# Kernel tuning notes

Hardware: AMD Instinct MI355X
Metric: run time of the kernel (lower is better)

Reference implementation:

```python
import jax, jax.numpy as jnp
import numpy as np

K = 4  # neighbors per node (loop=False, PyG knn_graph default)

def _leaky(x):
    return jax.nn.leaky_relu(x, negative_slope=0.01)

def _knn(pos):
    # pos: [B, N, 3]. k nearest neighbors per node within its own graph, no self-loops.
    d = jnp.sum((pos[:, :, None, :] - pos[:, None, :, :]) ** 2, axis=-1)  # [B, N, N]
    n = pos.shape[1]
    d = jnp.where(jnp.eye(n, dtype=bool), jnp.inf, d)
    _, idx = jax.lax.top_k(-d, K)
    return idx  # [B, N, K] neighbor (source) indices per center node

def _edge_conv(x, idx, w1, b1, w2, b2):
    # PyG EdgeConv, aggr='add': out_i = sum_j MLP(concat[x_i, x_j - x_i])
    xj = jax.vmap(lambda xb, ib: xb[ib])(x, idx)  # gather neighbors -> [B, N, K, F]
    xi = x[:, :, None, :]
    e = jnp.concatenate([jnp.broadcast_to(xi, xj.shape), xj - xi], axis=-1)  # [B,N,K,2F]
    h = _leaky(_leaky(e @ w1 + b1) @ w2 + b2)
    return h.sum(axis=2)  # scatter-add over the K neighbors -> [B, N, F_out]

# l1=4, l2=96, l3=192, l4=252, l5=192, l6=96, l7=1  (input_size=4, c=3, output_size=1)
PARAM_SHAPES = [
    ("c1w1", (8, 96)), ("c1b1", (96,)), ("c1w2", (96, 192)), ("c1b2", (192,)),
    ("c2w1", (384, 252)), ("c2b1", (252,)), ("c2w2", (252, 192)), ("c2b2", (192,)),
    ("c3w1", (384, 252)), ("c3b1", (252,)), ("c3w2", (252, 192)), ("c3b2", (192,)),
    ("c4w1", (384, 252)), ("c4b1", (252,)), ("c4w2", (252, 192)), ("c4b2", (192,)),
    ("nn1w", (772, 252)), ("nn1b", (252,)),
    ("nn2w", (252, 192)), ("nn2b", (192,)),
    ("nn3w", (768, 96)), ("nn3b", (96,)),
    ("nn4w", (96, 1)), ("nn4b", (1,)),
]

def setup_inputs():
    key = jax.random.key(0)
    B, N, F = 256, 256, 4  # 256 graphs x 256 nodes, 4 node features
    inp = {"x": jax.random.normal(key, (B, N, F), jnp.float32)}
    for i, (name, shp) in enumerate(PARAM_SHAPES):
        k = jax.random.fold_in(key, i + 1)
        scale = 1.0 / np.sqrt(shp[0]) if len(shp) == 2 else 0.01
        inp[name] = jax.random.normal(k, shp, jnp.float32) * scale
    return inp

def reference(x, c1w1, c1b1, c1w2, c1b2, c2w1, c2b1, c2w2, c2b2,
              c3w1, c3b1, c3w2, c3b2, c4w1, c4b1, c4w2, c4b2,
              nn1w, nn1b, nn2w, nn2b, nn3w, nn3b, nn4w, nn4b):
    # 4 rounds of (dynamic kNN on first 3 feature cols) + EdgeConv(add)
    a = _edge_conv(x, _knn(x[..., :3]), c1w1, c1b1, c1w2, c1b2)
    b = _edge_conv(a, _knn(a[..., :3]), c2w1, c2b1, c2w2, c2b2)
    c = _edge_conv(b, _knn(b[..., :3]), c3w1, c3b1, c3w2, c3b2)
    d = _edge_conv(c, _knn(c[..., :3]), c4w1, c4b1, c4w2, c4b2)
    h = jnp.concatenate([x, a, b, c, d], axis=-1)  # [B, N, 4 + 4*192 = 772]
    h = _leaky(h @ nn1w + nn1b)
    h = h @ nn2w + nn2b  # [B, N, 192]
    # four-way global pooling per graph: max / min / sum / mean
    pooled = jnp.concatenate(
        [h.max(axis=1), h.min(axis=1), h.sum(axis=1), h.mean(axis=1)], axis=-1)  # [B, 768]
    out = _leaky(pooled)
    out = _leaky(out @ nn3w + nn3b)
    return out @ nn4w + nn4b  # [B, 1] (mode='custom': no tanh)
```

## Files before the change

kernel.cpp:

```cpp
#include <hip/hip_runtime.h>
#include <cstdint>
#include <cstddef>

#define LK(x) ((x) > 0.f ? (x) : 0.01f * (x))

typedef _Float16 f16x8 __attribute__((ext_vector_type(8)));
typedef _Float16 f16x4 __attribute__((ext_vector_type(4)));
typedef float f32x4 __attribute__((ext_vector_type(4)));

constexpr int B_ = 256;
constexpr int N_ = 256;
constexpr int BN = B_ * N_;
constexpr int CHUNK_B = 64;
constexpr int CHUNK_ROWS = CHUNK_B * N_;

__device__ inline void dec2(float v, _Float16& h, _Float16& l) {
  _Float16 hh = (_Float16)v;
  h = hh;
  l = (_Float16)(v - (float)hh);
}

__global__ void knn_kernel(const float* __restrict__ feat, int F, int* __restrict__ idxout) {
  __shared__ float px[N_], py[N_], pz[N_];
  int b = blockIdx.x, t = threadIdx.x;
  const float* row = feat + ((size_t)b * N_ + t) * F;
  px[t] = row[0]; py[t] = row[1]; pz[t] = row[2];
  __syncthreads();
  float x = px[t], y = py[t], z = pz[t];
  float bd0 = INFINITY, bd1 = INFINITY, bd2 = INFINITY, bd3 = INFINITY;
  int bi0 = 0, bi1 = 0, bi2 = 0, bi3 = 0;
  for (int j = 0; j < N_; ++j) {
    #pragma clang fp contract(off)
    float dx = x - px[j], dy = y - py[j], dz = z - pz[j];
    float d = (dx * dx + dy * dy) + dz * dz;
    if (j == t) continue;
    if (d < bd3) {
      if (d < bd2) {
        bd3 = bd2; bi3 = bi2;
        if (d < bd1) {
          bd2 = bd1; bi2 = bi1;
          if (d < bd0) { bd1 = bd0; bi1 = bi0; bd0 = d; bi0 = j; }
          else         { bd1 = d; bi1 = j; }
        } else         { bd2 = d; bi2 = j; }
      } else           { bd3 = d; bi3 = j; }
    }
  }
  int* o = idxout + ((size_t)b * N_ + t) * 4;
  o[0] = bi0; o[1] = bi1; o[2] = bi2; o[3] = bi3;
}


__global__ void prep_uvw(const float* __restrict__ w1, const float* __restrict__ b1,
                         int F, int H1, float* __restrict__ wcat, float* __restrict__ bcat) {
  int t = blockIdx.x * 256 + threadIdx.x;
  int FH = F * H1;
  if (t < FH) {
    int k = t / H1, c = t - k * H1;
    float top = w1[(size_t)k * H1 + c];
    float bot = w1[(size_t)(F + k) * H1 + c];
    wcat[(size_t)k * 2 * H1 + c]      = top - bot;
    wcat[(size_t)k * 2 * H1 + H1 + c] = bot;
  }
  if (t < H1) { bcat[t] = b1[t]; bcat[H1 + t] = 0.f; }
}

template<bool ACT_A, bool ACCUM, bool HAS_BIAS>
__global__ __launch_bounds__(256) void gemm_f32(
    const float* __restrict__ A, const float* __restrict__ W,
    const float* __restrict__ bias, float* __restrict__ C,
    int M, int N, int K) {
  __shared__ float sA[16][132];
  __shared__ float sW[16][132];
  int tid = threadIdx.x;
  int m0 = blockIdx.y * 128;
  int n0 = blockIdx.x * 128;
  int kkA = tid & 15, mA = tid >> 4;
  int nW = tid & 127, kW = tid >> 7;
  int ty = tid >> 4, tx = tid & 15;
  float acc[8][8] = {};
  for (int k0 = 0; k0 < K; k0 += 16) {
    int kg = k0 + kkA;
    #pragma unroll
    for (int i = 0; i < 8; ++i) {
      int m = mA + i * 16;
      float v = 0.f;
      if (kg < K) {
        v = A[(size_t)(m0 + m) * K + kg];
        if (ACT_A) v = LK(v);
      }
      sA[kkA][m] = v;
    }
    #pragma unroll
    for (int q = 0; q < 8; ++q) {
      int kk = kW + q * 2;
      int kgw = k0 + kk, n = n0 + nW;
      float v = 0.f;
      if (kgw < K && n < N) v = W[(size_t)kgw * N + n];
      sW[kk][nW] = v;
    }
    __syncthreads();
    #pragma unroll
    for (int kk = 0; kk < 16; ++kk) {
      float4 a0 = *(const float4*)&sA[kk][ty * 8];
      float4 a1 = *(const float4*)&sA[kk][ty * 8 + 4];
      float4 w0 = *(const float4*)&sW[kk][tx * 4];
      float4 w1 = *(const float4*)&sW[kk][64 + tx * 4];
      float av[8] = {a0.x, a0.y, a0.z, a0.w, a1.x, a1.y, a1.z, a1.w};
      float wv[8] = {w0.x, w0.y, w0.z, w0.w, w1.x, w1.y, w1.z, w1.w};
      #pragma unroll
      for (int i = 0; i < 8; ++i)
        #pragma unroll
        for (int j = 0; j < 8; ++j)
          acc[i][j] += av[i] * wv[j];
    }
    __syncthreads();
  }
  #pragma unroll
  for (int h = 0; h < 2; ++h) {
    int n = n0 + h * 64 + tx * 4;
    float bv[4] = {0.f, 0.f, 0.f, 0.f};
    if (HAS_BIAS) {
      #pragma unroll
      for (int j = 0; j < 4; ++j) if (n + j < N) bv[j] = bias[n + j];
    }
    #pragma unroll
    for (int i = 0; i < 8; ++i) {
      size_t m = (size_t)(m0 + ty * 8 + i);
      if (n + 3 < N) {
        float4 o;
        o.x = acc[i][h * 4 + 0] + bv[0]; o.y = acc[i][h * 4 + 1] + bv[1];
        o.z = acc[i][h * 4 + 2] + bv[2]; o.w = acc[i][h * 4 + 3] + bv[3];
        float4* cp = (float4*)(C + m * N + n);
        if (ACCUM) { float4 c = *cp; o.x += c.x; o.y += c.y; o.z += c.z; o.w += c.w; }
        *cp = o;
      } else {
        #pragma unroll
        for (int j = 0; j < 4; ++j) {
          if (n + j < N) {
            float v = acc[i][h * 4 + j] + bv[j];
            size_t off = m * N + n + j;
            if (ACCUM) v += C[off];
            C[off] = v;
          }
        }
      }
    }
  }
}

__global__ __launch_bounds__(256) void edge_stage2(
    const float* __restrict__ UV, const int* __restrict__ idx,
    const float* __restrict__ w2, const float* __restrict__ b2,
    float* __restrict__ out, int H1) {
  __shared__ float sH[16][68];
  __shared__ float sW[16][196];
  __shared__ int sJ[64];
  int tid = threadIdx.x;
  int g0 = blockIdx.x * 16;
  int bbase = (g0 >> 8) << 8;
  if (tid < 64) sJ[tid] = bbase + idx[(size_t)g0 * 4 + tid];
  int W2 = H1 * 2;
  int r = tid >> 2, seg = tid & 3;
  int gp_r = g0 + (r >> 2);
  int ty = tid >> 4, tx = tid & 15;
  int gp = g0 + ty;
  float acc[4][12] = {};
  int nKt = (H1 + 15) >> 4;
  for (int kt = 0; kt < nKt; ++kt) {
    int k0 = kt << 4;
    __syncthreads();
    {
      int c = k0 + (seg << 2);
      const float* up = UV + (size_t)gp_r * W2 + c;
      const float* vp = UV + (size_t)sJ[r] * W2 + H1 + c;
      float u[4], v[4];
      if (c + 3 < H1) {
        float4 uu = *(const float4*)up; float4 vv = *(const float4*)vp;
        u[0] = uu.x; u[1] = uu.y; u[2] = uu.z; u[3] = uu.w;
        v[0] = vv.x; v[1] = vv.y; v[2] = vv.z; v[3] = vv.w;
      } else {
        #pragma unroll
        for (int j = 0; j < 4; ++j) {
          u[j] = (c + j < H1) ? up[j] : 0.f;
          v[j] = (c + j < H1) ? vp[j] : 0.f;
        }
      }
      #pragma unroll
      for (int j = 0; j < 4; ++j) {
        float t = u[j] + v[j];
        sH[(seg << 2) + j][r] = (c + j < H1) ? LK(t) : 0.f;
      }
    }
    #pragma unroll
    for (int p = 0; p < 3; ++p) {
      int q = tid + (p << 8);
      int kk = q / 48;
      int c4 = q - kk * 48;
      int k = k0 + kk;
      float4 wv = {0.f, 0.f, 0.f, 0.f};
      if (k < H1) wv = *(const float4*)(w2 + (size_t)k * 192 + (c4 << 2));
      *(float4*)&sW[kk][c4 << 2] = wv;
    }
    __syncthreads();
    #pragma unroll
    for (int kk = 0; kk < 16; ++kk) {
      float4 a = *(const float4*)&sH[kk][ty << 2];
      float av[4] = {a.x, a.y, a.z, a.w};
      #pragma unroll
      for (int ct = 0; ct < 3; ++ct) {
        float4 w = *(const float4*)&sW[kk][ct * 64 + (tx << 2)];
        float wv[4] = {w.x, w.y, w.z, w.w};
        #pragma unroll
        for (int i = 0; i < 4; ++i)
          #pragma unroll
          for (int j = 0; j < 4; ++j)
            acc[i][ct * 4 + j] += av[i] * wv[j];
      }
    }
  }
  #pragma unroll
  for (int ct = 0; ct < 3; ++ct) {
    float o[4];
    #pragma unroll
    for (int j = 0; j < 4; ++j) {
      int col = ct * 64 + (tx << 2) + j;
      float bvv = b2[col];
      float s = 0.f;
      #pragma unroll
      for (int i = 0; i < 4; ++i) {
        float t = acc[i][ct * 4 + j] + bvv;
        s += LK(t);
      }
      o[j] = s;
    }
    float4 ov = {o[0], o[1], o[2], o[3]};
    *(float4*)(out + (size_t)gp * 192 + ct * 64 + (tx << 2)) = ov;
  }
}

__global__ __launch_bounds__(256) void edge_exact3(
    const float* __restrict__ UV, const int* __restrict__ idx,
    const float* __restrict__ w2, const float* __restrict__ b2,
    float* __restrict__ out, int H1) {
  __shared__ float sw[252 * 4];
  int tid = threadIdx.x;
  for (int k = tid; k < H1; k += 256) {
    sw[k * 4 + 0] = w2[(size_t)k * 192 + 0];
    sw[k * 4 + 1] = w2[(size_t)k * 192 + 1];
    sw[k * 4 + 2] = w2[(size_t)k * 192 + 2];
    sw[k * 4 + 3] = 0.f;
  }
  __syncthreads();
  int p = blockIdx.x * 64 + (tid >> 2);
  int e = tid & 3;
  int bbase = (p >> 8) << 8;
  int j = bbase + idx[(size_t)p * 4 + e];
  int W2 = 2 * H1;
  const float* up = UV + (size_t)p * W2;
  const float* vp = UV + (size_t)j * W2 + H1;
  float a0 = 0.f, a1 = 0.f, a2 = 0.f;
  int k = 0;
  for (; k + 3 < H1; k += 4) {
    float4 u = *(const float4*)(up + k);
    float4 v = *(const float4*)(vp + k);
    float h0 = LK(u.x + v.x), h1 = LK(u.y + v.y);
    float h2 = LK(u.z + v.z), h3 = LK(u.w + v.w);
    float4 w0 = *(const float4*)&sw[(k + 0) * 4];
    float4 w1 = *(const float4*)&sw[(k + 1) * 4];
    float4 w2v = *(const float4*)&sw[(k + 2) * 4];
    float4 w3 = *(const float4*)&sw[(k + 3) * 4];
    a0 = __builtin_fmaf(h0, w0.x, a0); a1 = __builtin_fmaf(h0, w0.y, a1); a2 = __builtin_fmaf(h0, w0.z, a2);
    a0 = __builtin_fmaf(h1, w1.x, a0); a1 = __builtin_fmaf(h1, w1.y, a1); a2 = __builtin_fmaf(h1, w1.z, a2);
    a0 = __builtin_fmaf(h2, w2v.x, a0); a1 = __builtin_fmaf(h2, w2v.y, a1); a2 = __builtin_fmaf(h2, w2v.z, a2);
    a0 = __builtin_fmaf(h3, w3.x, a0); a1 = __builtin_fmaf(h3, w3.y, a1); a2 = __builtin_fmaf(h3, w3.z, a2);
  }
  for (; k < H1; ++k) {
    float h = LK(up[k] + vp[k]);
    a0 = __builtin_fmaf(h, sw[k * 4 + 0], a0);
    a1 = __builtin_fmaf(h, sw[k * 4 + 1], a1);
    a2 = __builtin_fmaf(h, sw[k * 4 + 2], a2);
  }
  float acc3[3] = {a0, a1, a2};
  #pragma unroll
  for (int c = 0; c < 3; ++c) {
    float t = acc3[c] + b2[c];
    float pc = LK(t);
    float q1 = __shfl_down(pc, 1);
    float q2 = __shfl_down(pc, 2);
    float q3 = __shfl_down(pc, 3);
    if (e == 0) {
      float s = ((pc + q1) + q2) + q3;
      out[(size_t)p * 192 + c] = s;
    }
  }
}


__global__ void prep_wcatT(const float* __restrict__ w1, const float* __restrict__ b1,
                           int F, int H1, int Fpad, _Float16* __restrict__ Wp,
                           float* __restrict__ bcat) {
  int t = blockIdx.x * 256 + threadIdx.x;
  int NN = 2 * H1;
  if (t < NN * Fpad) {
    int n = t / Fpad, k = t - n * Fpad;
    float v = 0.f;
    if (k < F) {
      if (n < H1) v = w1[(size_t)k * H1 + n] - w1[(size_t)(F + k) * H1 + n];
      else        v = w1[(size_t)(F + k) * H1 + (n - H1)];
    }
    _Float16 h, l; dec2(v, h, l);
    size_t base = (size_t)n * 2 * Fpad + (size_t)(k >> 3) * 16 + (k & 7);
    Wp[base] = h; Wp[base + 8] = l;
  }
  if (t < NN) bcat[t] = (t < H1) ? b1[t] : 0.f;
}

__global__ void prep_wT(const float* __restrict__ W, int K, int N, int Kpad,
                        _Float16* __restrict__ Wp) {
  int t = blockIdx.x * 256 + threadIdx.x;
  if (t >= N * Kpad) return;
  int n = t / Kpad, k = t - n * Kpad;
  float v = (k < K) ? W[(size_t)k * N + n] : 0.f;
  _Float16 h, l; dec2(v, h, l);
  size_t base = (size_t)n * 2 * Kpad + (size_t)(k >> 3) * 16 + (k & 7);
  Wp[base] = h; Wp[base + 8] = l;
}

template<bool ACT_A, bool ACCUM, bool HAS_BIAS, bool XB>
__global__ __launch_bounds__(256) void gemm3h(
    const float* __restrict__ A0, const float* __restrict__ A1, int w0,
    const _Float16* __restrict__ Wp, const float* __restrict__ bias,
    const float* __restrict__ X, const float* __restrict__ Wx,
    float* __restrict__ C, int M, int N, int K, int Kpad) {
  __shared__ _Float16 sA[128 * 72];
  __shared__ _Float16 sB[128 * 72];
  int tid = threadIdx.x;
  int m0 = blockIdx.y * 128, n0 = blockIdx.x * 128;
  int lane = tid & 63, wid = tid >> 6;
  int wy = wid >> 1, wx = wid & 1;
  int lm = lane & 15, lq = lane >> 4;
  int rA = tid >> 1, qA = (tid & 1) * 4;
  f32x4 acc[4][4];
  #pragma unroll
  for (int i = 0; i < 4; ++i)
    #pragma unroll
    for (int j = 0; j < 4; ++j) acc[i][j] = 0.f;

  for (int k0 = 0; k0 < Kpad; k0 += 32) {
    __syncthreads();
    {
      const float* Ap; int kb, wA;
      if (k0 < w0) { Ap = A0; kb = k0;      wA = w0; }
      else         { Ap = A1; kb = k0 - w0; wA = K - w0; }
      const float* arow = Ap + (size_t)(m0 + rA) * wA;
      #pragma unroll
      for (int qi = 0; qi < 4; ++qi) {
        int q = qA + qi;
        int kl = kb + q * 4;
        float4 v = {0.f, 0.f, 0.f, 0.f};
        if (kl + 3 < wA) v = *(const float4*)(arow + kl);
        else {
          if (kl + 0 < wA) v.x = arow[kl + 0];
          if (kl + 1 < wA) v.y = arow[kl + 1];
          if (kl + 2 < wA) v.z = arow[kl + 2];
        }
        if (ACT_A) { v.x = LK(v.x); v.y = LK(v.y); v.z = LK(v.z); v.w = LK(v.w); }
        _Float16 h0,h1,h2,h3,l0,l1,l2,l3;
        dec2(v.x,h0,l0); dec2(v.y,h1,l1); dec2(v.z,h2,l2); dec2(v.w,h3,l3);
        int off = rA * 72 + (q >> 1) * 16 + (q & 1) * 4;
        f16x4 th; th[0]=h0; th[1]=h1; th[2]=h2; th[3]=h3;
        f16x4 tl; tl[0]=l0; tl[1]=l1; tl[2]=l2; tl[3]=l3;
        *(f16x4*)&sA[off]     = th;
        *(f16x4*)&sA[off + 8] = tl;
      }
    }
    {
      int n = n0 + rA;
      const _Float16* src = Wp + (size_t)n * 2 * Kpad + (size_t)k0 * 2;
      #pragma unroll
      for (int ui = 0; ui < 4; ++ui) {
        int u = (tid & 1) * 4 + ui;
        float4 v = {0.f, 0.f, 0.f, 0.f};
        if (n < N) v = *(const float4*)(src + u * 8);
        *(float4*)&sB[rA * 72 + u * 8] = v;
      }
    }
    __syncthreads();
    f16x8 af[4][2], bf[4][2];
    #pragma unroll
    for (int mt = 0; mt < 4; ++mt) {
      int row = wy * 64 + mt * 16 + lm;
      af[mt][0] = *(const f16x8*)&sA[row * 72 + lq * 16];
      af[mt][1] = *(const f16x8*)&sA[row * 72 + lq * 16 + 8];
    }
    #pragma unroll
    for (int nt = 0; nt < 4; ++nt) {
      int row = wx * 64 + nt * 16 + lm;
      bf[nt][0] = *(const f16x8*)&sB[row * 72 + lq * 16];
      bf[nt][1] = *(const f16x8*)&sB[row * 72 + lq * 16 + 8];
    }
    #pragma unroll
    for (int mt = 0; mt < 4; ++mt)
      #pragma unroll
      for (int nt = 0; nt < 4; ++nt) {
        acc[mt][nt] = __builtin_amdgcn_mfma_f32_16x16x32_f16(af[mt][0], bf[nt][0], acc[mt][nt], 0, 0, 0);
        acc[mt][nt] = __builtin_amdgcn_mfma_f32_16x16x32_f16(af[mt][0], bf[nt][1], acc[mt][nt], 0, 0, 0);
        acc[mt][nt] = __builtin_amdgcn_mfma_f32_16x16x32_f16(af[mt][1], bf[nt][0], acc[mt][nt], 0, 0, 0);
      }
  }
  if (XB) {
    #pragma unroll
    for (int mt = 0; mt < 4; ++mt) {
      #pragma unroll
      for (int r = 0; r < 4; ++r) {
        size_t m = (size_t)m0 + wy * 64 + mt * 16 + lq * 4 + r;
        float4 xv = *(const float4*)(X + m * 4);
        #pragma unroll
        for (int nt = 0; nt < 4; ++nt) {
          int n = n0 + wx * 64 + nt * 16 + lm;
          if (n >= N) continue;
          float v = acc[mt][nt][r] + bias[n]
                  + (xv.x * Wx[n] + xv.y * Wx[N + n] + xv.z * Wx[2 * N + n] + xv.w * Wx[3 * N + n]);
          C[m * N + n] = v;
        }
      }
    }
    return;
  }
  #pragma unroll
  for (int mt = 0; mt < 4; ++mt) {
    #pragma unroll
    for (int nt = 0; nt < 4; ++nt) {
      int n = n0 + wx * 64 + nt * 16 + lm;
      if (n >= N) continue;
      float bv = HAS_BIAS ? bias[n] : 0.f;
      #pragma unroll
      for (int r = 0; r < 4; ++r) {
        size_t m = (size_t)m0 + wy * 64 + mt * 16 + lq * 4 + r;
        float v = acc[mt][nt][r] + bv;
        size_t off = m * N + n;
        if (ACCUM) v += C[off];
        C[off] = v;
      }
    }
  }
}

__global__ __launch_bounds__(256) void edge_stage2_m(
    const float* __restrict__ UV, const int* __restrict__ idx,
    const _Float16* __restrict__ Wp, const float* __restrict__ b2,
    float* __restrict__ out, int H1, int Kpad) {
  __shared__ _Float16 sH[64 * 72];
  __shared__ _Float16 sW[192 * 72];
  __shared__ int sJ[64];
  int tid = threadIdx.x;
  int g0 = blockIdx.x * 16;
  int bbase = (g0 >> 8) << 8;
  if (tid < 64) sJ[tid] = bbase + idx[(size_t)g0 * 4 + tid];
  int W2 = 2 * H1;
  int lane = tid & 63, w = tid >> 6;
  int lm = lane & 15, lq = lane >> 4;
  int rS = tid >> 2, qS = tid & 3;
  f32x4 acc[4][3];
  #pragma unroll
  for (int i = 0; i < 4; ++i)
    #pragma unroll
    for (int j = 0; j < 3; ++j) acc[i][j] = 0.f;

  for (int k0 = 0; k0 < Kpad; k0 += 32) {
    __syncthreads();
    {
      int gp_r = g0 + (rS >> 2);
      int jr = sJ[rS];
      const float* up = UV + (size_t)gp_r * W2;
      const float* vp = UV + (size_t)jr * W2 + H1;
      #pragma unroll
      for (int hf = 0; hf < 2; ++hf) {
        int k = k0 + qS * 8 + hf * 4;
        float4 u = {0.f,0.f,0.f,0.f}, v = {0.f,0.f,0.f,0.f};
        if (k + 3 < H1) { u = *(const float4*)(up + k); v = *(const float4*)(vp + k); }
        else {
          if (k + 0 < H1) { u.x = up[k+0]; v.x = vp[k+0]; }
          if (k + 1 < H1) { u.y = up[k+1]; v.y = vp[k+1]; }
          if (k + 2 < H1) { u.z = up[k+2]; v.z = vp[k+2]; }
        }
        float e0 = LK(u.x + v.x), e1 = LK(u.y + v.y), e2 = LK(u.z + v.z), e3 = LK(u.w + v.w);
        _Float16 h0,h1,h2,h3,l0,l1,l2,l3;
        dec2(e0,h0,l0); dec2(e1,h1,l1); dec2(e2,h2,l2); dec2(e3,h3,l3);
        int off = rS * 72 + qS * 16 + hf * 4;
        f16x4 th; th[0]=h0; th[1]=h1; th[2]=h2; th[3]=h3;
        f16x4 tl; tl[0]=l0; tl[1]=l1; tl[2]=l2; tl[3]=l3;
        *(f16x4*)&sH[off]     = th;
        *(f16x4*)&sH[off + 8] = tl;
      }
    }
    {
      const _Float16* src = Wp + (size_t)k0 * 2;
      #pragma unroll
      for (int p = 0; p < 6; ++p) {
        int e = tid + p * 256;
        int n = e >> 3, u = e & 7;
        *(float4*)&sW[n * 72 + u * 8] =
            *(const float4*)(src + (size_t)n * 2 * Kpad + u * 8);
      }
    }
    __syncthreads();
    f16x8 af[4][2], bf[3][2];
    #pragma unroll
    for (int mt = 0; mt < 4; ++mt) {
      int row = mt * 16 + lm;
      af[mt][0] = *(const f16x8*)&sH[row * 72 + lq * 16];
      af[mt][1] = *(const f16x8*)&sH[row * 72 + lq * 16 + 8];
    }
    #pragma unroll
    for (int t3 = 0; t3 < 3; ++t3) {
      int row = (w * 3 + t3) * 16 + lm;
      bf[t3][0] = *(const f16x8*)&sW[row * 72 + lq * 16];
      bf[t3][1] = *(const f16x8*)&sW[row * 72 + lq * 16 + 8];
    }
    #pragma unroll
    for (int mt = 0; mt < 4; ++mt)
      #pragma unroll
      for (int t3 = 0; t3 < 3; ++t3) {
        acc[mt][t3] = __builtin_amdgcn_mfma_f32_16x16x32_f16(af[mt][0], bf[t3][0], acc[mt][t3], 0, 0, 0);
        acc[mt][t3] = __builtin_amdgcn_mfma_f32_16x16x32_f16(af[mt][0], bf[t3][1], acc[mt][t3], 0, 0, 0);
        acc[mt][t3] = __builtin_amdgcn_mfma_f32_16x16x32_f16(af[mt][1], bf[t3][0], acc[mt][t3], 0, 0, 0);
      }
  }
  #pragma unroll
  for (int mt = 0; mt < 4; ++mt) {
    int gp = g0 + mt * 4 + lq;
    #pragma unroll
    for (int t3 = 0; t3 < 3; ++t3) {
      int col = (w * 3 + t3) * 16 + lm;
      float bv = b2[col];
      float s = 0.f;
      #pragma unroll
      for (int r = 0; r < 4; ++r) s += LK(acc[mt][t3][r] + bv);
      out[(size_t)gp * 192 + col] = s;
    }
  }
}

__global__ void pool_kernel(const float* __restrict__ h, float* __restrict__ pooled) {
  int b = blockIdx.x, ch = threadIdx.x;
  const float* p = h + (size_t)b * N_ * 192 + ch;
  float mx = -INFINITY, mn = INFINITY, sm = 0.f;
  for (int n = 0; n < N_; ++n) {
    float v = p[(size_t)n * 192];
    mx = fmaxf(mx, v); mn = fminf(mn, v); sm += v;
  }
  float* o = pooled + (size_t)b * 768;
  o[ch]       = LK(mx);
  o[192 + ch] = LK(mn);
  o[384 + ch] = LK(sm);
  o[576 + ch] = LK(sm * (1.f / 256.f));
}

__global__ void head_kernel(const float* __restrict__ pooled,
                            const float* __restrict__ w3, const float* __restrict__ b3,
                            const float* __restrict__ w4, const float* __restrict__ b4,
                            float* __restrict__ out) {
  __shared__ float sp[768];
  __shared__ float st[96];
  int b = blockIdx.x, t = threadIdx.x;
  for (int c = t; c < 768; c += 128) sp[c] = pooled[(size_t)b * 768 + c];
  __syncthreads();
  if (t < 96) {
    float s = b3[t];
    for (int r = 0; r < 768; ++r) s += sp[r] * w3[(size_t)r * 96 + t];
    s = LK(s);
    st[t] = s * w4[t];
  }
  __syncthreads();
  if (t == 0) {
    float s = b4[0];
    for (int i = 0; i < 96; ++i) s += st[i];
    out[b] = s;
  }
}

extern "C" void kernel_launch(void* const* d_in, const int* in_sizes, int n_in,
                              void* d_out, int out_size, void* d_ws, size_t ws_size,
                              hipStream_t stream) {
  (void)in_sizes; (void)n_in; (void)out_size; (void)ws_size;
  const float* x = (const float*)d_in[0];
  const float* P[25];
  for (int i = 0; i < 25; ++i) P[i] = (const float*)d_in[i];

  char* ws = (char*)d_ws;
  int*   idx    = (int*)  (ws + 0);
  float* A      = (float*)(ws + 1048576);
  float* Bb     = (float*)(ws + 51380224);
  float* h1     = (float*)(ws + 101711872);
  float* UV     = (float*)(ws + 167772160);
  float* pooled = (float*)(ws + 200802304);
  char*  Wsl1   =         (ws + 201588736);
  char*  Wsl2   =         (ws + 202637312);
  float* bcat   = (float*)(ws + 203685888);

  float*    wcat = (float*)   Wsl1;
  _Float16* WB1  = (_Float16*)Wsl1;
  _Float16* WB2  = (_Float16*)Wsl2;

  auto edge_layer_f32 = [&](const float* src, int F, int H1,
                            const float* w1, const float* b1,
                            const float* w2, const float* b2, float* dst) {
    knn_kernel<<<B_, N_, 0, stream>>>(src, F, idx);
    prep_uvw<<<(F * H1 + 255) / 256, 256, 0, stream>>>(w1, b1, F, H1, wcat, bcat);
    int W2 = 2 * H1;
    dim3 gUV((W2 + 127) / 128, CHUNK_ROWS / 128);
    for (int cb = 0; cb < B_; cb += CHUNK_B) {
      size_t base = (size_t)cb * N_;
      gemm_f32<false, false, true><<<gUV, 256, 0, stream>>>(src + base * F, wcat, bcat, UV, CHUNK_ROWS, W2, F);
      edge_stage2<<<CHUNK_ROWS / 16, 256, 0, stream>>>(UV, idx + base * 4, w2, b2, dst + base * 192, H1);
    }
  };

  auto edge_layer_f16 = [&](const float* src, int F, int H1,
                            const float* w1, const float* b1,
                            const float* w2, const float* b2, float* dst) {
    int Fpad = (F + 31) & ~31;
    int KpadW2 = (H1 + 31) & ~31;
    int NN = 2 * H1;
    knn_kernel<<<B_, N_, 0, stream>>>(src, F, idx);
    prep_wcatT<<<(NN * Fpad + 255) / 256, 256, 0, stream>>>(w1, b1, F, H1, Fpad, WB1, bcat);
    prep_wT<<<(192 * KpadW2 + 255) / 256, 256, 0, stream>>>(w2, H1, 192, KpadW2, WB2);
    dim3 gUV((NN + 127) / 128, CHUNK_ROWS / 128);
    for (int cb = 0; cb < B_; cb += CHUNK_B) {
      size_t base = (size_t)cb * N_;
      gemm3h<false, false, true, false><<<gUV, 256, 0, stream>>>(
          src + base * F, src + base * F, F, WB1, bcat, nullptr, nullptr, UV, CHUNK_ROWS, NN, F, Fpad);
      edge_stage2_m<<<CHUNK_ROWS / 16, 256, 0, stream>>>(
          UV, idx + base * 4, WB2, b2, dst + base * 192, H1, KpadW2);
    }
  };

  edge_layer_f32(x,  4,   96,  P[1], P[2], P[3], P[4], A);
  edge_layer_f32(A,  192, 252, P[5], P[6], P[7], P[8], Bb);

  {
    prep_wT<<<(252 * 384 + 255) / 256, 256, 0, stream>>>(P[17] + 4 * 252, 384, 252, 384, WB1);
    dim3 g(2, BN / 128);
    gemm3h<false, false, true, true><<<g, 256, 0, stream>>>(
        A, Bb, 192, WB1, P[18], x, P[17], h1, BN, 252, 384, 384);
  }

  {
    const float* src = Bb;
    const float* w1 = P[9]; const float* b1 = P[10];
    const float* w2 = P[11]; const float* b2 = P[12];
    float* dst = A;
    int F = 192, H1 = 252, W2 = 504, KpadW2 = 256;
    knn_kernel<<<B_, N_, 0, stream>>>(src, F, idx);
    prep_uvw<<<(F * H1 + 255) / 256, 256, 0, stream>>>(w1, b1, F, H1, wcat, bcat);
    prep_wT<<<(192 * KpadW2 + 255) / 256, 256, 0, stream>>>(w2, H1, 192, KpadW2, WB2);
    dim3 gUV((W2 + 127) / 128, CHUNK_ROWS / 128);
    for (int cb = 0; cb < B_; cb += CHUNK_B) {
      size_t base = (size_t)cb * N_;
      gemm_f32<false, false, true><<<gUV, 256, 0, stream>>>(src + base * F, wcat, bcat, UV, CHUNK_ROWS, W2, F);
      edge_stage2_m<<<CHUNK_ROWS / 16, 256, 0, stream>>>(UV, idx + base * 4, WB2, b2, dst + base * 192, H1, KpadW2);
      edge_exact3<<<CHUNK_ROWS / 64, 256, 0, stream>>>(UV, idx + base * 4, w2, b2, dst + base * 192, H1);
    }
  }

  edge_layer_f16(A, 192, 252, P[13], P[14], P[15], P[16], Bb);

  {
    prep_wT<<<(252 * 384 + 255) / 256, 256, 0, stream>>>(P[17] + (size_t)388 * 252, 384, 252, 384, WB1);
    dim3 g(2, BN / 128);
    gemm3h<false, true, false, false><<<g, 256, 0, stream>>>(
        A, Bb, 192, WB1, nullptr, nullptr, nullptr, h1, BN, 252, 384, 384);
  }

  {
    prep_wT<<<(192 * 256 + 255) / 256, 256, 0, stream>>>(P[19], 252, 192, 256, WB2);
    dim3 g(2, BN / 128);
    gemm3h<true, false, true, false><<<g, 256, 0, stream>>>(
        h1, h1, 252, WB2, P[20], nullptr, nullptr, A, BN, 192, 252, 256);
  }

  pool_kernel<<<B_, 192, 0, stream>>>(A, pooled);
  head_kernel<<<B_, 128, 0, stream>>>(pooled, P[21], P[22], P[23], P[24], (float*)d_out);
}
```

Before: 2.175 ms.

## Narrow f32 GEMM tile to 64 columns and register-prefetch gemm3h operands

Measured after the change: 2.017 ms. 7.3% less time.

```diff
diff --git a/kernel.cpp b/kernel.cpp
--- a/kernel.cpp
+++ b/kernel.cpp
@@ -70,14 +70,14 @@
     const float* __restrict__ bias, float* __restrict__ C,
     int M, int N, int K) {
   __shared__ float sA[16][132];
-  __shared__ float sW[16][132];
+  __shared__ float sW[16][68];
   int tid = threadIdx.x;
   int m0 = blockIdx.y * 128;
-  int n0 = blockIdx.x * 128;
+  int n0 = blockIdx.x * 64;
   int kkA = tid & 15, mA = tid >> 4;
-  int nW = tid & 127, kW = tid >> 7;
+  int nW = tid & 63, kW = tid >> 6;
   int ty = tid >> 4, tx = tid & 15;
-  float acc[8][8] = {};
+  float acc[8][4] = {};
   for (int k0 = 0; k0 < K; k0 += 16) {
     int kg = k0 + kkA;
     #pragma unroll
@@ -91,8 +91,8 @@
       sA[kkA][m] = v;
     }
     #pragma unroll
-    for (int q = 0; q < 8; ++q) {
-      int kk = kW + q * 2;
+    for (int q = 0; q < 4; ++q) {
+      int kk = kW + q * 4;
       int kgw = k0 + kk, n = n0 + nW;
       float v = 0.f;
       if (kgw < K && n < N) v = W[(size_t)kgw * N + n];
@@ -103,45 +103,41 @@
     for (int kk = 0; kk < 16; ++kk) {
       float4 a0 = *(const float4*)&sA[kk][ty * 8];
       float4 a1 = *(const float4*)&sA[kk][ty * 8 + 4];
-      float4 w0 = *(const float4*)&sW[kk][tx * 4];
-      float4 w1 = *(const float4*)&sW[kk][64 + tx * 4];
+      float4 w  = *(const float4*)&sW[kk][tx * 4];
       float av[8] = {a0.x, a0.y, a0.z, a0.w, a1.x, a1.y, a1.z, a1.w};
-      float wv[8] = {w0.x, w0.y, w0.z, w0.w, w1.x, w1.y, w1.z, w1.w};
+      float wv[4] = {w.x, w.y, w.z, w.w};
       #pragma unroll
       for (int i = 0; i < 8; ++i)
         #pragma unroll
-        for (int j = 0; j < 8; ++j)
+        for (int j = 0; j < 4; ++j)
           acc[i][j] += av[i] * wv[j];
     }
     __syncthreads();
   }
+  int n = n0 + tx * 4;
+  float bv[4] = {0.f, 0.f, 0.f, 0.f};
+  if (HAS_BIAS) {
+    #pragma unroll
+    for (int j = 0; j < 4; ++j) if (n + j < N) bv[j] = bias[n + j];
+  }
   #pragma unroll
-  for (int h = 0; h < 2; ++h) {
-    int n = n0 + h * 64 + tx * 4;
-    float bv[4] = {0.f, 0.f, 0.f, 0.f};
-    if (HAS_BIAS) {
-      #pragma unroll
-      for (int j = 0; j < 4; ++j) if (n + j < N) bv[j] = bias[n + j];
-    }
-    #pragma unroll
-    for (int i = 0; i < 8; ++i) {
-      size_t m = (size_t)(m0 + ty * 8 + i);
-      if (n + 3 < N) {
-        float4 o;
-        o.x = acc[i][h * 4 + 0] + bv[0]; o.y = acc[i][h * 4 + 1] + bv[1];
-        o.z = acc[i][h * 4 + 2] + bv[2]; o.w = acc[i][h * 4 + 3] + bv[3];
-        float4* cp = (float4*)(C + m * N + n);
-        if (ACCUM) { float4 c = *cp; o.x += c.x; o.y += c.y; o.z += c.z; o.w += c.w; }
-        *cp = o;
-      } else {
-        #pragma unroll
-        for (int j = 0; j < 4; ++j) {
-          if (n + j < N) {
-            float v = acc[i][h * 4 + j] + bv[j];
-            size_t off = m * N + n + j;
-            if (ACCUM) v += C[off];
-            C[off] = v;
-          }
+  for (int i = 0; i < 8; ++i) {
+    size_t m = (size_t)(m0 + ty * 8 + i);
+    if (n + 3 < N) {
+      float4 o;
+      o.x = acc[i][0] + bv[0]; o.y = acc[i][1] + bv[1];
+      o.z = acc[i][2] + bv[2]; o.w = acc[i][3] + bv[3];
+      float4* cp = (float4*)(C + m * N + n);
+      if (ACCUM) { float4 c = *cp; o.x += c.x; o.y += c.y; o.z += c.z; o.w += c.w; }
+      *cp = o;
+    } else {
+      #pragma unroll
+      for (int j = 0; j < 4; ++j) {
+        if (n + j < N) {
+          float v = acc[i][j] + bv[j];
+          size_t off = m * N + n + j;
+          if (ACCUM) v += C[off];
+          C[off] = v;
         }
       }
     }
@@ -346,45 +342,63 @@
     #pragma unroll
     for (int j = 0; j < 4; ++j) acc[i][j] = 0.f;
 
+  float4 pa0, pa1, pa2, pa3, pb0, pb1, pb2, pb3;
+
+#define LOADA_ONE(KL, DST)                                          \
+  { int kl_ = (KL); float4 v_ = {0.f, 0.f, 0.f, 0.f};               \
+    if (kl_ + 3 < wA) v_ = *(const float4*)(arow + kl_);            \
+    else {                                                          \
+      if (kl_ + 0 < wA) v_.x = arow[kl_ + 0];                       \
+      if (kl_ + 1 < wA) v_.y = arow[kl_ + 1];                       \
+      if (kl_ + 2 < wA) v_.z = arow[kl_ + 2]; }                     \
+    DST = v_; }
+
+#define LOAD_AB(K0)                                                 \
+  { int k0_ = (K0);                                                 \
+    const float* Ap; int kb, wA;                                    \
+    if (k0_ < w0) { Ap = A0; kb = k0_;      wA = w0; }              \
+    else          { Ap = A1; kb = k0_ - w0; wA = K - w0; }          \
+    const float* arow = Ap + (size_t)(m0 + rA) * wA;                \
+    LOADA_ONE(kb + (qA + 0) * 4, pa0)                               \
+    LOADA_ONE(kb + (qA + 1) * 4, pa1)                               \
+    LOADA_ONE(kb + (qA + 2) * 4, pa2)                               \
+    LOADA_ONE(kb + (qA + 3) * 4, pa3)                               \
+    int n_ = n0 + rA;                                               \
+    const _Float16* src = Wp + (size_t)n_ * 2 * Kpad + (size_t)k0_ * 2; \
+    float4 z_ = {0.f, 0.f, 0.f, 0.f};                               \
+    if (n_ < N) {                                                   \
+      pb0 = *(const float4*)(src + (qA + 0) * 8);                   \
+      pb1 = *(const float4*)(src + (qA + 1) * 8);                   \
+      pb2 = *(const float4*)(src + (qA + 2) * 8);                   \
+      pb3 = *(const float4*)(src + (qA + 3) * 8);                   \
+    } else { pb0 = z_; pb1 = z_; pb2 = z_; pb3 = z_; } }
+
+#define ST_A(V, Q)                                                  \
+  { float4 t_ = (V);                                                \
+    if (ACT_A) { t_.x = LK(t_.x); t_.y = LK(t_.y);                  \
+                 t_.z = LK(t_.z); t_.w = LK(t_.w); }                \
+    _Float16 h0,h1,h2,h3,l0,l1,l2,l3;                               \
+    dec2(t_.x,h0,l0); dec2(t_.y,h1,l1);                             \
+    dec2(t_.z,h2,l2); dec2(t_.w,h3,l3);                             \
+    int off_ = rA * 72 + ((Q) >> 1) * 16 + ((Q) & 1) * 4;           \
+    f16x4 th; th[0]=h0; th[1]=h1; th[2]=h2; th[3]=h3;               \
+    f16x4 tl; tl[0]=l0; tl[1]=l1; tl[2]=l2; tl[3]=l3;               \
+    *(f16x4*)&sA[off_]     = th;                                    \
+    *(f16x4*)&sA[off_ + 8] = tl; }
+
+  LOAD_AB(0)
+
   for (int k0 = 0; k0 < Kpad; k0 += 32) {
     __syncthreads();
-    {
-      const float* Ap; int kb, wA;
-      if (k0 < w0) { Ap = A0; kb = k0;      wA = w0; }
-      else         { Ap = A1; kb = k0 - w0; wA = K - w0; }
-      const float* arow = Ap + (size_t)(m0 + rA) * wA;
-      #pragma unroll
-      for (int qi = 0; qi < 4; ++qi) {
-        int q = qA + qi;
-        int kl = kb + q * 4;
-        float4 v = {0.f, 0.f, 0.f, 0.f};
-        if (kl + 3 < wA) v = *(const float4*)(arow + kl);
-        else {
-          if (kl + 0 < wA) v.x = arow[kl + 0];
-          if (kl + 1 < wA) v.y = arow[kl + 1];
-          if (kl + 2 < wA) v.z = arow[kl + 2];
-        }
-        if (ACT_A) { v.x = LK(v.x); v.y = LK(v.y); v.z = LK(v.z); v.w = LK(v.w); }
-        _Float16 h0,h1,h2,h3,l0,l1,l2,l3;
-        dec2(v.x,h0,l0); dec2(v.y,h1,l1); dec2(v.z,h2,l2); dec2(v.w,h3,l3);
-        int off = rA * 72 + (q >> 1) * 16 + (q & 1) * 4;
-        f16x4 th; th[0]=h0; th[1]=h1; th[2]=h2; th[3]=h3;
-        f16x4 tl; tl[0]=l0; tl[1]=l1; tl[2]=l2; tl[3]=l3;
-        *(f16x4*)&sA[off]     = th;
-        *(f16x4*)&sA[off + 8] = tl;
-      }
-    }
-    {
-      int n = n0 + rA;
-      const _Float16* src = Wp + (size_t)n * 2 * Kpad + (size_t)k0 * 2;
-      #pragma unroll
-      for (int ui = 0; ui < 4; ++ui) {
-        int u = (tid & 1) * 4 + ui;
-        float4 v = {0.f, 0.f, 0.f, 0.f};
-        if (n < N) v = *(const float4*)(src + u * 8);
-        *(float4*)&sB[rA * 72 + u * 8] = v;
-      }
-    }
+    ST_A(pa0, qA + 0)
+    ST_A(pa1, qA + 1)
+    ST_A(pa2, qA + 2)
+    ST_A(pa3, qA + 3)
+    *(float4*)&sB[rA * 72 + (qA + 0) * 8] = pb0;
+    *(float4*)&sB[rA * 72 + (qA + 1) * 8] = pb1;
+    *(float4*)&sB[rA * 72 + (qA + 2) * 8] = pb2;
+    *(float4*)&sB[rA * 72 + (qA + 3) * 8] = pb3;
+    if (k0 + 32 < Kpad) { LOAD_AB(k0 + 32) }
     __syncthreads();
     f16x8 af[4][2], bf[4][2];
     #pragma unroll
@@ -408,6 +422,9 @@
         acc[mt][nt] = __builtin_amdgcn_mfma_f32_16x16x32_f16(af[mt][1], bf[nt][0], acc[mt][nt], 0, 0, 0);
       }
   }
+#undef LOADA_ONE
+#undef LOAD_AB
+#undef ST_A
   if (XB) {
     #pragma unroll
     for (int mt = 0; mt < 4; ++mt) {
@@ -609,7 +626,7 @@
     knn_kernel<<<B_, N_, 0, stream>>>(src, F, idx);
     prep_uvw<<<(F * H1 + 255) / 256, 256, 0, stream>>>(w1, b1, F, H1, wcat, bcat);
     int W2 = 2 * H1;
-    dim3 gUV((W2 + 127) / 128, CHUNK_ROWS / 128);
+    dim3 gUV((W2 + 63) / 64, CHUNK_ROWS / 128);
     for (int cb = 0; cb < B_; cb += CHUNK_B) {
       size_t base = (size_t)cb * N_;
       gemm_f32<false, false, true><<<gUV, 256, 0, stream>>>(src + base * F, wcat, bcat, UV, CHUNK_ROWS, W2, F);
@@ -655,7 +672,7 @@
     knn_kernel<<<B_, N_, 0, stream>>>(src, F, idx);
     prep_uvw<<<(F * H1 + 255) / 256, 256, 0, stream>>>(w1, b1, F, H1, wcat, bcat);
     prep_wT<<<(192 * KpadW2 + 255) / 256, 256, 0, stream>>>(w2, H1, 192, KpadW2, WB2);
-    dim3 gUV((W2 + 127) / 128, CHUNK_ROWS / 128);
+    dim3 gUV((W2 + 63) / 64, CHUNK_ROWS / 128);
     for (int cb = 0; cb < B_; cb += CHUNK_B) {
       size_t base = (size_t)cb * N_;
       gemm_f32<false, false, true><<<gUV, 256, 0, stream>>>(src + base * F, wcat, bcat, UV, CHUNK_ROWS, W2, F);
```
